# Performance work log

Measured on AMD Instinct MI355X. Metric: run time of the kernel, lower is better.

## Reference

```python
import jax, jax.numpy as jnp
import numpy as np

B, N, HIDDEN, N_HEADS, N_EDGE = 2, 1024, 512, 8, 16
HEAD_DIM = HIDDEN // N_HEADS


def setup_inputs() -> dict:
    key = jax.random.key(0)
    ks = jax.random.split(key, 12)
    s = 1.0 / np.sqrt(HIDDEN)
    se = 1.0 / np.sqrt(N_EDGE)
    return {
        "x": jax.random.normal(ks[0], (B, N, HIDDEN), jnp.float32),
        "edge_features": jax.random.normal(ks[1], (B, N, N, N_EDGE), jnp.float32),
        "attn_mask": jax.random.randint(ks[2], (B, N, N), 0, 2) == 1,
        # projections stored (in, out)
        "Wq": jax.random.uniform(ks[3], (HIDDEN, HIDDEN), jnp.float32, -s, s),
        "bq": jnp.zeros((HIDDEN,), jnp.float32),
        "Wk": jax.random.uniform(ks[4], (HIDDEN, HIDDEN), jnp.float32, -s, s),
        "bk": jnp.zeros((HIDDEN,), jnp.float32),
        "Wv": jax.random.uniform(ks[5], (HIDDEN, HIDDEN), jnp.float32, -s, s),
        "bv": jnp.zeros((HIDDEN,), jnp.float32),
        "Wo": jax.random.uniform(ks[6], (HIDDEN, HIDDEN), jnp.float32, -s, s),
        "bo": jnp.zeros((HIDDEN,), jnp.float32),
        # edge-bias MLP: n_edge_features -> 2*n_heads -(ELU)-> n_heads
        "We1": jax.random.uniform(ks[7], (N_EDGE, 2 * N_HEADS), jnp.float32, -se, se),
        "be1": jnp.zeros((2 * N_HEADS,), jnp.float32),
        "We2": jax.random.uniform(ks[8], (2 * N_HEADS, N_HEADS), jnp.float32, -0.25, 0.25),
        "be2": jnp.zeros((N_HEADS,), jnp.float32),
    }


def reference(x, edge_features, attn_mask, Wq, bq, Wk, bk, Wv, bv, Wo, bo, We1, be1, We2, be2):
    Bv, Nv, _ = x.shape
    scale = jnp.asarray(np.sqrt(HEAD_DIM), x.dtype)
    # projections -> (B, H, N, D)
    q = (x @ Wq + bq).reshape(Bv, Nv, N_HEADS, HEAD_DIM).transpose(0, 2, 1, 3)
    k = (x @ Wk + bk).reshape(Bv, Nv, N_HEADS, HEAD_DIM).transpose(0, 2, 1, 3)
    v = (x @ Wv + bv).reshape(Bv, Nv, N_HEADS, HEAD_DIM).transpose(0, 2, 1, 3)
    attn = jnp.einsum("bhqd,bhkd->bhqk", q, k) / scale
    # per-edge MLP bias: (B, N, N, F) -> (B, N, N, H) -> (B, H, N, N)
    e_h = jax.nn.elu(edge_features @ We1 + be1)
    e_bias = (e_h @ We2 + be2).transpose(0, 3, 1, 2)
    attn = attn + e_bias
    attn = jnp.where(attn_mask[:, None, :, :], -jnp.inf, attn)
    attn = jax.nn.softmax(attn, axis=-1)
    attn = jnp.nan_to_num(attn, nan=0.0)  # fully-masked rows -> 0
    # dropout is identity in eval mode
    out = jnp.einsum("bhqk,bhkd->bqhd", attn, v).reshape(Bv, Nv, HIDDEN)
    return out @ Wo + bo, attn
```

## Files before the change

### kernel.cpp

```cpp
#include <hip/hip_runtime.h>

#define NB 2
#define NN 1024
#define HID 512
#define NHD 8
#define HD 64
#define NE 16

typedef float f4 __attribute__((ext_vector_type(4)));
typedef float f2 __attribute__((ext_vector_type(2)));

__global__ __launch_bounds__(256) void k_maskdet(const unsigned int* __restrict__ m,
                                                 int* __restrict__ flag) {
    __shared__ int sh;
    if (threadIdx.x == 0) sh = 0;
    __syncthreads();
    int loc = 0;
    for (int i = threadIdx.x; i < 4096; i += 256) {
        unsigned v = m[i];
        if (v == 0x3F800000u) loc |= 1;
        else if (v > 1u) loc |= 2;
        else if (v != 0u) loc |= (i & 1) ? 4 : 8;
    }
    if (loc) atomicOr(&sh, loc);
    __syncthreads();
    if (threadIdx.x == 0) {
        int s = sh;
        int mode;
        if (s & 1) mode = 2;
        else if (s & 2) mode = 1;
        else if ((s & 8) && !(s & 4)) mode = 3;
        else mode = 0;
        *flag = mode;
    }
}

__device__ __forceinline__ float eluf(float x) {
    return x > 0.f ? x : (__expf(x) - 1.f);
}

__device__ __forceinline__ void gemm_tile_512(
    const float* __restrict__ X, const float* __restrict__ W,
    int m0, int n0, float* xs, float4 acc[4]) {
    int tid = threadIdx.x;
    int tn = tid & 15, tm = tid >> 4;
    acc[0] = make_float4(0.f, 0.f, 0.f, 0.f);
    acc[1] = acc[0]; acc[2] = acc[0]; acc[3] = acc[0];
    for (int kc = 0; kc < 512; kc += 64) {
        __syncthreads();
#pragma unroll
        for (int j = 0; j < 4; j++) {
            int ml = tm + 16 * j;
            *(float4*)(xs + ml * 64 + tn * 4) =
                *(const float4*)(X + (size_t)(m0 + ml) * 512 + kc + tn * 4);
        }
        __syncthreads();
#pragma unroll 4
        for (int k4 = 0; k4 < 16; k4++) {
            float4 x0 = *(const float4*)(xs + (tm * 4 + 0) * 64 + k4 * 4);
            float4 x1 = *(const float4*)(xs + (tm * 4 + 1) * 64 + k4 * 4);
            float4 x2 = *(const float4*)(xs + (tm * 4 + 2) * 64 + k4 * 4);
            float4 x3 = *(const float4*)(xs + (tm * 4 + 3) * 64 + k4 * 4);
            const float* wr = W + (size_t)(kc + k4 * 4) * 512 + n0 + tn * 4;
#pragma unroll
            for (int kk = 0; kk < 4; kk++) {
                float4 w = *(const float4*)(wr + (size_t)kk * 512);
                float a0 = (kk == 0) ? x0.x : (kk == 1) ? x0.y : (kk == 2) ? x0.z : x0.w;
                float a1 = (kk == 0) ? x1.x : (kk == 1) ? x1.y : (kk == 2) ? x1.z : x1.w;
                float a2 = (kk == 0) ? x2.x : (kk == 1) ? x2.y : (kk == 2) ? x2.z : x2.w;
                float a3 = (kk == 0) ? x3.x : (kk == 1) ? x3.y : (kk == 2) ? x3.z : x3.w;
                acc[0].x += a0 * w.x; acc[0].y += a0 * w.y; acc[0].z += a0 * w.z; acc[0].w += a0 * w.w;
                acc[1].x += a1 * w.x; acc[1].y += a1 * w.y; acc[1].z += a1 * w.z; acc[1].w += a1 * w.w;
                acc[2].x += a2 * w.x; acc[2].y += a2 * w.y; acc[2].z += a2 * w.z; acc[2].w += a2 * w.w;
                acc[3].x += a3 * w.x; acc[3].y += a3 * w.y; acc[3].z += a3 * w.z; acc[3].w += a3 * w.w;
            }
        }
    }
}

__global__ __launch_bounds__(256) void k_qkv_t(
    const float* __restrict__ x,
    const float* __restrict__ Wq, const float* __restrict__ Wk, const float* __restrict__ Wv,
    const float* __restrict__ bq, const float* __restrict__ bk, const float* __restrict__ bv,
    float* __restrict__ qb, float* __restrict__ kt, float* __restrict__ vb) {
    __shared__ __align__(16) float xs[64 * 64];
    int bx = blockIdx.x;
    int which = bx >> 8; bx &= 255;
    int m0 = (bx >> 3) * 64, n0 = (bx & 7) * 64;
    const float* W    = (which == 0) ? Wq : (which == 1) ? Wk : Wv;
    const float* bias = (which == 0) ? bq : (which == 1) ? bk : bv;
    float4 acc[4];
    gemm_tile_512(x, W, m0, n0, xs, acc);
    int tn = threadIdx.x & 15, tm = threadIdx.x >> 4;
    float4 bv4 = *(const float4*)(bias + n0 + tn * 4);
    int hh = n0 >> 6, d = tn * 4;
#pragma unroll
    for (int r = 0; r < 4; r++) {
        int m = m0 + tm * 4 + r;
        int b = m >> 10, tok = m & 1023;
        float4 v = acc[r];
        v.x += bv4.x; v.y += bv4.y; v.z += bv4.z; v.w += bv4.w;
        if (which == 1) {
            float* kth = kt + (size_t)(b * NHD + hh) * (HD * NN);
            kth[(size_t)(d + 0) * NN + tok] = v.x;
            kth[(size_t)(d + 1) * NN + tok] = v.y;
            kth[(size_t)(d + 2) * NN + tok] = v.z;
            kth[(size_t)(d + 3) * NN + tok] = v.w;
        } else {
            float* out = (which == 0) ? qb : vb;
            *(float4*)(out + (((size_t)(b * NHD + hh) * NN + tok) * HD + d)) = v;
        }
    }
}

#define QK2(QV, A0, A1)                                                        \
    A0 = fmaf(QV.x, k0v.x, fmaf(QV.y, k1v.x, fmaf(QV.z, k2v.x, fmaf(QV.w, k3v.x, A0)))); \
    A1 = fmaf(QV.x, k0v.y, fmaf(QV.y, k1v.y, fmaf(QV.z, k2v.y, fmaf(QV.w, k3v.y, A1))));

#define DOT16(E, R)                                                            \
    fmaf(E[15], wD.w, fmaf(E[14], wD.z, fmaf(E[13], wD.y, fmaf(E[12], wD.x,    \
    fmaf(E[11], wC.w, fmaf(E[10], wC.z, fmaf(E[9],  wC.y, fmaf(E[8],  wC.x,    \
    fmaf(E[7],  wB.w, fmaf(E[6],  wB.z, fmaf(E[5],  wB.y, fmaf(E[4],  wB.x,    \
    fmaf(E[3],  wA.w, fmaf(E[2],  wA.z, fmaf(E[1],  wA.y, fmaf(E[0],  wA.x, R))))))))))))))))

__global__ __launch_bounds__(512, 2) void k_fscore(
    const float* __restrict__ qb, const float* __restrict__ kt,
    const float* __restrict__ ef,
    const float* __restrict__ We1, const float* __restrict__ be1,
    const float* __restrict__ We2, const float* __restrict__ be2,
    const void* __restrict__ mask, const int* __restrict__ mode_p,
    float* __restrict__ attn) {
    __shared__ __align__(16) float w1t[16][16];
    __shared__ __align__(16) float w2[16][8];
    __shared__ __align__(16) float b1s[16];
    __shared__ __align__(16) float b2s[8];
    __shared__ __align__(16) float qs[8][4][64];
    __shared__ __align__(16) float biasS[8][4][128];
    int tid = threadIdx.x;
    if (tid < 256) w1t[tid & 15][tid >> 4] = We1[tid];
    else if (tid < 384) { int u = tid - 256; w2[u >> 3][u & 7] = We2[u]; }
    else if (tid < 400) b1s[tid - 384] = be1[tid - 384];
    else if (tid < 408) b2s[tid - 400] = be2[tid - 400];

    int bid = blockIdx.x;
    int lb = (bid & 7) * 64 + (bid >> 3);
    int b = lb >> 8, q0 = (lb & 255) * 4;

    {
        int h = tid >> 6, q = (tid >> 4) & 3, c = tid & 15;
        *(float4*)(&qs[h][q][4 * c]) =
            *(const float4*)(qb + (((size_t)(b * NHD + h) * NN + q0 + q) * HD + 4 * c));
    }
    __syncthreads();
    int mode = *mode_p;
    int wv = tid >> 6, lane = tid & 63;
    const float* kth = kt + (size_t)(b * NHD + wv) * (HD * NN);
    int mq = tid >> 7, mk = tid & 127;
    const float* efq = ef + (((size_t)b * NN) + q0 + mq) * (NN * NE);
    size_t mrow = (((size_t)b * NN) + q0 + mq) * NN;
    size_t arow = ((size_t)(b * NHD + wv) * NN + q0) * NN;

    for (int t = 0; t < 8; t++) {
        int k0 = t * 128 + mk;
        {
            float e0[16];
            {
                const f4* pe0 = (const f4*)(efq + (size_t)k0 * NE);
#pragma unroll
                for (int c = 0; c < 4; c++) {
                    f4 v0 = __builtin_nontemporal_load(pe0 + c);
                    e0[4*c+0]=v0.x; e0[4*c+1]=v0.y; e0[4*c+2]=v0.z; e0[4*c+3]=v0.w;
                }
            }
            float acc0[8];
#pragma unroll
            for (int j = 0; j < 8; j++) acc0[j] = b2s[j];
#pragma unroll 2
            for (int o = 0; o < 16; o++) {
                float4 wA = *(const float4*)(&w1t[o][0]);
                float4 wB = *(const float4*)(&w1t[o][4]);
                float4 wC = *(const float4*)(&w1t[o][8]);
                float4 wD = *(const float4*)(&w1t[o][12]);
                float a0 = DOT16(e0, b1s[o]);
                float g0v = eluf(a0);
                float4 u0 = *(const float4*)(&w2[o][0]);
                float4 u1 = *(const float4*)(&w2[o][4]);
                acc0[0] = fmaf(g0v, u0.x, acc0[0]); acc0[1] = fmaf(g0v, u0.y, acc0[1]);
                acc0[2] = fmaf(g0v, u0.z, acc0[2]); acc0[3] = fmaf(g0v, u0.w, acc0[3]);
                acc0[4] = fmaf(g0v, u1.x, acc0[4]); acc0[5] = fmaf(g0v, u1.y, acc0[5]);
                acc0[6] = fmaf(g0v, u1.z, acc0[6]); acc0[7] = fmaf(g0v, u1.w, acc0[7]);
            }
            size_t p0i = mrow + k0;
            bool m0;
            if (mode == 3)      m0 = ((const unsigned int*)mask)[2 * p0i] != 0u;
            else if (mode == 2) m0 = ((const float*)mask)[p0i] != 0.0f;
            else if (mode == 1) m0 = ((const unsigned char*)mask)[p0i] != 0;
            else                m0 = ((const int*)mask)[p0i] != 0;
#pragma unroll
            for (int hh = 0; hh < 8; hh++)
                biasS[hh][mq][mk] = m0 ? -1e30f : acc0[hh];
        }
        __syncthreads();
        {
            float a00=0.f,a01=0.f, a10=0.f,a11=0.f, a20=0.f,a21=0.f, a30=0.f,a31=0.f;
            const float* kb0 = kth + t * 128 + 2 * lane;
#pragma unroll 2
            for (int dc = 0; dc < 16; dc++) {
                float4 qv0 = *(const float4*)(&qs[wv][0][dc * 4]);
                float4 qv1 = *(const float4*)(&qs[wv][1][dc * 4]);
                float4 qv2 = *(const float4*)(&qs[wv][2][dc * 4]);
                float4 qv3 = *(const float4*)(&qs[wv][3][dc * 4]);
                float2 k0v = *(const float2*)(kb0 + (size_t)(dc * 4 + 0) * NN);
                float2 k1v = *(const float2*)(kb0 + (size_t)(dc * 4 + 1) * NN);
                float2 k2v = *(const float2*)(kb0 + (size_t)(dc * 4 + 2) * NN);
                float2 k3v = *(const float2*)(kb0 + (size_t)(dc * 4 + 3) * NN);
                QK2(qv0, a00, a01);
                QK2(qv1, a10, a11);
                QK2(qv2, a20, a21);
                QK2(qv3, a30, a31);
            }
            float2 b0 = *(const float2*)(&biasS[wv][0][2 * lane]);
            float2 b1 = *(const float2*)(&biasS[wv][1][2 * lane]);
            float2 b2 = *(const float2*)(&biasS[wv][2][2 * lane]);
            float2 b3 = *(const float2*)(&biasS[wv][3][2 * lane]);
            f2 p0, p1, p2, p3;
            p0.x = __expf(fmaf(a00, 0.125f, b0.x)); p0.y = __expf(fmaf(a01, 0.125f, b0.y));
            p1.x = __expf(fmaf(a10, 0.125f, b1.x)); p1.y = __expf(fmaf(a11, 0.125f, b1.y));
            p2.x = __expf(fmaf(a20, 0.125f, b2.x)); p2.y = __expf(fmaf(a21, 0.125f, b2.y));
            p3.x = __expf(fmaf(a30, 0.125f, b3.x)); p3.y = __expf(fmaf(a31, 0.125f, b3.y));
            size_t kc = (size_t)t * 128 + 2 * lane;
            *(f2*)(attn + arow + 0 * NN + kc) = p0;
            *(f2*)(attn + arow + 1 * NN + kc) = p1;
            *(f2*)(attn + arow + 2 * NN + kc) = p2;
            *(f2*)(attn + arow + 3 * NN + kc) = p3;
        }
        __syncthreads();
    }
}

__global__ __launch_bounds__(256) void k_av2(
    float* __restrict__ attn, const float* __restrict__ vb,
    float* __restrict__ oattn) {
    int bid = blockIdx.x;
    int lb = (bid & 7) * 128 + (bid >> 3);
    int w = lb * 4 + (threadIdx.x >> 6);
    int lane = threadIdx.x & 63;
    int bh = w >> 8;
    int q0 = (w & 255) * 4;
    float* ar = attn + ((size_t)bh * NN + q0) * NN;
    const float* vbh = vb + (size_t)bh * (NN * HD);
    float acc[4] = {0.f, 0.f, 0.f, 0.f};
    float sum[4] = {0.f, 0.f, 0.f, 0.f};
#pragma unroll 2
    for (int k = 0; k < NN; k += 4) {
        float4 a[4];
#pragma unroll
        for (int r = 0; r < 4; r++) a[r] = *(const float4*)(ar + (size_t)r * NN + k);
        float v0 = vbh[(k + 0) * HD + lane];
        float v1 = vbh[(k + 1) * HD + lane];
        float v2 = vbh[(k + 2) * HD + lane];
        float v3 = vbh[(k + 3) * HD + lane];
#pragma unroll
        for (int r = 0; r < 4; r++) {
            acc[r] += a[r].x * v0;
            acc[r] += a[r].y * v1;
            acc[r] += a[r].z * v2;
            acc[r] += a[r].w * v3;
            sum[r] += (a[r].x + a[r].y) + (a[r].z + a[r].w);
        }
    }
    int b = bh >> 3, hh = bh & 7;
#pragma unroll
    for (int r = 0; r < 4; r++) {
        float inv = (sum[r] > 0.f) ? 1.f / sum[r] : 0.f;
        oattn[(size_t)(b * NN + q0 + r) * HID + hh * 64 + lane] = acc[r] * inv;
        float* row = ar + (size_t)r * NN;
#pragma unroll
        for (int k = 4 * lane; k < NN; k += 256) {
            float4 v = *(const float4*)(row + k);
            v.x *= inv; v.y *= inv; v.z *= inv; v.w *= inv;
            *(float4*)(row + k) = v;
        }
    }
}

__global__ __launch_bounds__(256) void k_oproj_t(
    const float* __restrict__ oa, const float* __restrict__ Wo,
    const float* __restrict__ bo, float* __restrict__ out) {
    __shared__ __align__(16) float xs[64 * 64];
    int bx = blockIdx.x;
    int m0 = (bx >> 3) * 64, n0 = (bx & 7) * 64;
    float4 acc[4];
    gemm_tile_512(oa, Wo, m0, n0, xs, acc);
    int tn = threadIdx.x & 15, tm = threadIdx.x >> 4;
    float4 bv4 = *(const float4*)(bo + n0 + tn * 4);
#pragma unroll
    for (int r = 0; r < 4; r++) {
        int m = m0 + tm * 4 + r;
        float4 v = acc[r];
        v.x += bv4.x; v.y += bv4.y; v.z += bv4.z; v.w += bv4.w;
        *(float4*)(out + (size_t)m * HID + n0 + tn * 4) = v;
    }
}

extern "C" void kernel_launch(void* const* d_in, const int* in_sizes, int n_in,
                              void* d_out, int out_size, void* d_ws, size_t ws_size,
                              hipStream_t stream) {
    (void)in_sizes; (void)n_in; (void)out_size; (void)ws_size;
    const float* x   = (const float*)d_in[0];
    const float* ef  = (const float*)d_in[1];
    const void*  msk = d_in[2];
    const float* Wq  = (const float*)d_in[3];
    const float* bq  = (const float*)d_in[4];
    const float* Wk  = (const float*)d_in[5];
    const float* bk  = (const float*)d_in[6];
    const float* Wv  = (const float*)d_in[7];
    const float* bv  = (const float*)d_in[8];
    const float* Wo  = (const float*)d_in[9];
    const float* bo  = (const float*)d_in[10];
    const float* We1 = (const float*)d_in[11];
    const float* be1 = (const float*)d_in[12];
    const float* We2 = (const float*)d_in[13];
    const float* be2 = (const float*)d_in[14];

    char* ws = (char*)d_ws;
    float* qb    = (float*)(ws + 0);
    float* kt    = (float*)(ws + 4194304);
    float* vb    = (float*)(ws + 8388608);
    float* oattn = (float*)(ws + 12582912);
    int*   flag  = (int*)(ws + 16777216);

    float* out0 = (float*)d_out;
    float* attn = out0 + (size_t)NB * NN * HID;

    k_maskdet<<<1, 256, 0, stream>>>((const unsigned int*)msk, flag);
    k_qkv_t<<<768, 256, 0, stream>>>(x, Wq, Wk, Wv, bq, bk, bv, qb, kt, vb);
    k_fscore<<<512, 512, 0, stream>>>(qb, kt, ef, We1, be1, We2, be2, msk, flag, attn);
    k_av2<<<1024, 256, 0, stream>>>(attn, vb, oattn);
    k_oproj_t<<<256, 256, 0, stream>>>(oattn, Wo, bo, out0);
}
```

Baseline: 654.6 us.

## Compute softmax row sums in score kernel and halve rows per AV warp

The score kernel now accumulates the exponentiated scores per query row, reduces them across the wavefront with shuffles, and writes the row sums to a new workspace buffer. The AV kernel reads these sums instead of recomputing them, and each wavefront now handles 2 query rows instead of 4, so twice as many blocks are launched. This removes the per-element sum additions from the AV kernel and raises parallelism. The cost is fewer rows sharing each V load, so V traffic per output rises, plus a small extra reduction and write in the score kernel.

```diff
diff --git a/kernel.cpp b/kernel.cpp
--- a/kernel.cpp
+++ b/kernel.cpp
@@ -129,7 +129,7 @@
     const float* __restrict__ We1, const float* __restrict__ be1,
     const float* __restrict__ We2, const float* __restrict__ be2,
     const void* __restrict__ mask, const int* __restrict__ mode_p,
-    float* __restrict__ attn) {
+    float* __restrict__ attn, float* __restrict__ sums) {
     __shared__ __align__(16) float w1t[16][16];
     __shared__ __align__(16) float w2[16][8];
     __shared__ __align__(16) float b1s[16];
@@ -159,6 +159,7 @@
     const float* efq = ef + (((size_t)b * NN) + q0 + mq) * (NN * NE);
     size_t mrow = (((size_t)b * NN) + q0 + mq) * NN;
     size_t arow = ((size_t)(b * NHD + wv) * NN + q0) * NN;
+    float psum0 = 0.f, psum1 = 0.f, psum2 = 0.f, psum3 = 0.f;
 
     for (int t = 0; t < 8; t++) {
         int k0 = t * 128 + mk;
@@ -228,6 +229,10 @@
             p1.x = __expf(fmaf(a10, 0.125f, b1.x)); p1.y = __expf(fmaf(a11, 0.125f, b1.y));
             p2.x = __expf(fmaf(a20, 0.125f, b2.x)); p2.y = __expf(fmaf(a21, 0.125f, b2.y));
             p3.x = __expf(fmaf(a30, 0.125f, b3.x)); p3.y = __expf(fmaf(a31, 0.125f, b3.y));
+            psum0 += p0.x + p0.y;
+            psum1 += p1.x + p1.y;
+            psum2 += p2.x + p2.y;
+            psum3 += p3.x + p3.y;
             size_t kc = (size_t)t * 128 + 2 * lane;
             *(f2*)(attn + arow + 0 * NN + kc) = p0;
             *(f2*)(attn + arow + 1 * NN + kc) = p1;
@@ -236,51 +241,57 @@
         }
         __syncthreads();
     }
+#pragma unroll
+    for (int off = 1; off < 64; off <<= 1) {
+        psum0 += __shfl_xor(psum0, off);
+        psum1 += __shfl_xor(psum1, off);
+        psum2 += __shfl_xor(psum2, off);
+        psum3 += __shfl_xor(psum3, off);
+    }
+    if (lane == 0) {
+        float* sr = sums + (((size_t)(b * NHD + wv)) << 10) + q0;
+        sr[0] = psum0; sr[1] = psum1; sr[2] = psum2; sr[3] = psum3;
+    }
 }
 
 __global__ __launch_bounds__(256) void k_av2(
     float* __restrict__ attn, const float* __restrict__ vb,
-    float* __restrict__ oattn) {
+    const float* __restrict__ sums, float* __restrict__ oattn) {
     int bid = blockIdx.x;
-    int lb = (bid & 7) * 128 + (bid >> 3);
+    int lb = (bid & 7) * 256 + (bid >> 3);
     int w = lb * 4 + (threadIdx.x >> 6);
     int lane = threadIdx.x & 63;
-    int bh = w >> 8;
-    int q0 = (w & 255) * 4;
+    int bh = w >> 9;
+    int q0 = (w & 511) * 2;
     float* ar = attn + ((size_t)bh * NN + q0) * NN;
     const float* vbh = vb + (size_t)bh * (NN * HD);
-    float acc[4] = {0.f, 0.f, 0.f, 0.f};
-    float sum[4] = {0.f, 0.f, 0.f, 0.f};
+    float s0 = sums[((size_t)bh << 10) + q0];
+    float s1 = sums[((size_t)bh << 10) + q0 + 1];
+    float inv0 = (s0 > 0.f) ? 1.f / s0 : 0.f;
+    float inv1 = (s1 > 0.f) ? 1.f / s1 : 0.f;
+    float acc0 = 0.f, acc1 = 0.f;
 #pragma unroll 2
     for (int k = 0; k < NN; k += 4) {
-        float4 a[4];
-#pragma unroll
-        for (int r = 0; r < 4; r++) a[r] = *(const float4*)(ar + (size_t)r * NN + k);
+        float4 a0 = *(const float4*)(ar + k);
+        float4 a1 = *(const float4*)(ar + NN + k);
         float v0 = vbh[(k + 0) * HD + lane];
         float v1 = vbh[(k + 1) * HD + lane];
         float v2 = vbh[(k + 2) * HD + lane];
         float v3 = vbh[(k + 3) * HD + lane];
-#pragma unroll
-        for (int r = 0; r < 4; r++) {
-            acc[r] += a[r].x * v0;
-            acc[r] += a[r].y * v1;
-            acc[r] += a[r].z * v2;
-            acc[r] += a[r].w * v3;
-            sum[r] += (a[r].x + a[r].y) + (a[r].z + a[r].w);
-        }
+        acc0 = fmaf(a0.x, v0, fmaf(a0.y, v1, fmaf(a0.z, v2, fmaf(a0.w, v3, acc0))));
+        acc1 = fmaf(a1.x, v0, fmaf(a1.y, v1, fmaf(a1.z, v2, fmaf(a1.w, v3, acc1))));
     }
     int b = bh >> 3, hh = bh & 7;
-#pragma unroll
-    for (int r = 0; r < 4; r++) {
-        float inv = (sum[r] > 0.f) ? 1.f / sum[r] : 0.f;
-        oattn[(size_t)(b * NN + q0 + r) * HID + hh * 64 + lane] = acc[r] * inv;
-        float* row = ar + (size_t)r * NN;
-#pragma unroll
-        for (int k = 4 * lane; k < NN; k += 256) {
-            float4 v = *(const float4*)(row + k);
-            v.x *= inv; v.y *= inv; v.z *= inv; v.w *= inv;
-            *(float4*)(row + k) = v;
-        }
+    oattn[(size_t)(b * NN + q0 + 0) * HID + hh * 64 + lane] = acc0 * inv0;
+    oattn[(size_t)(b * NN + q0 + 1) * HID + hh * 64 + lane] = acc1 * inv1;
+#pragma unroll
+    for (int k = 4 * lane; k < NN; k += 256) {
+        float4 v = *(const float4*)(ar + k);
+        v.x *= inv0; v.y *= inv0; v.z *= inv0; v.w *= inv0;
+        *(float4*)(ar + k) = v;
+        float4 u = *(const float4*)(ar + NN + k);
+        u.x *= inv1; u.y *= inv1; u.z *= inv1; u.w *= inv1;
+        *(float4*)(ar + NN + k) = u;
     }
 }
 
@@ -328,14 +339,15 @@
     float* kt    = (float*)(ws + 4194304);
     float* vb    = (float*)(ws + 8388608);
     float* oattn = (float*)(ws + 12582912);
-    int*   flag  = (int*)(ws + 16777216);
+    float* sums  = (float*)(ws + 16777216);
+    int*   flag  = (int*)(ws + 16842752);
 
     float* out0 = (float*)d_out;
     float* attn = out0 + (size_t)NB * NN * HID;
 
     k_maskdet<<<1, 256, 0, stream>>>((const unsigned int*)msk, flag);
     k_qkv_t<<<768, 256, 0, stream>>>(x, Wq, Wk, Wv, bq, bk, bv, qb, kt, vb);
-    k_fscore<<<512, 512, 0, stream>>>(qb, kt, ef, We1, be1, We2, be2, msk, flag, attn);
-    k_av2<<<1024, 256, 0, stream>>>(attn, vb, oattn);
+    k_fscore<<<512, 512, 0, stream>>>(qb, kt, ef, We1, be1, We2, be2, msk, flag, attn, sums);
+    k_av2<<<2048, 256, 0, stream>>>(attn, vb, sums, oattn);
     k_oproj_t<<<256, 256, 0, stream>>>(oattn, Wo, bo, out0);
 }
```

New measurement: 664.5 us. No clear change (+1.5%).
